# Performance work log

Measured on AMD Instinct MI355X. Metric: run time of the kernel, lower is better.

The kernel has to match this reference:

```python
import jax, jax.numpy as jnp
import numpy as np

MARGIN = 1.0
N, D = 4096, 512
NUM_CLASSES = 64


def setup_inputs() -> dict:
    key = jax.random.key(0)
    k1, k2 = jax.random.split(key)
    inputs = jax.random.normal(k1, (N, D), dtype=jnp.float32)
    targets = jax.random.randint(k2, (N,), 0, NUM_CLASSES, dtype=jnp.int64)
    return {"inputs": inputs, "targets": targets}


def reference(inputs, targets):
    n = inputs.shape[0]
    sq = jnp.sum(inputs * inputs, axis=1)  # [n]
    # squared Euclidean distances, clamped at 0 (matches relu in original)
    d2 = jnp.maximum(sq[:, None] + sq[None, :] - 2.0 * (inputs @ inputs.T), 0.0)
    # safe sqrt (zero entries get 0, matching forward; avoids NaN grads)
    dist = jnp.where(d2 > 0, jnp.sqrt(jnp.where(d2 > 0, d2, 1.0)), 0.0)  # [n,n]

    same = targets[:, None] == targets[None, :]
    eye = jnp.eye(n, dtype=bool)
    pos_mask = same & ~eye          # positives, diagonal excluded
    neg_mask = ~same                # negatives (diagonal is same-label, excluded)

    # per-row sum_k exp(margin - d_ik) over negatives  (replaces per-pair loop)
    neg_sum = jnp.sum(jnp.where(neg_mask, jnp.exp(MARGIN - dist), 0.0), axis=1)  # [n]

    # J_ij = log(neg_sum_i + neg_sum_j) + d_ij for positive pairs
    J = jnp.log(neg_sum[:, None] + neg_sum[None, :]) + dist
    triu_pos = jnp.triu(pos_mask)   # loop iterated over upper-triangular positives
    hinge2 = jnp.where(triu_pos, jax.nn.relu(J) ** 2, 0.0)

    # original divides by count of ALL positive entries (both triangles)
    len_p = jnp.sum(pos_mask).astype(jnp.float32)
    return jnp.sum(hinge2) / len_p
```

## Files before the change

### kernel.cpp

```cpp
#include <hip/hip_runtime.h>
#include <math.h>

#define NN 4096
#define DD 512
#define MARGINF 1.0f
#define NCLS 64
#define MAXM 160
#define TRI (MAXM * (MAXM - 1) / 2)
#define NBLK 2080

typedef __attribute__((ext_vector_type(8))) short bf16x8;
typedef __attribute__((ext_vector_type(4))) float f32x4;

#define WS_SQ   0
#define WS_LOSS 8192
#define WS_CTR  8193
#define WS_LENP 8194
#define WS_RK   8320
#define WS_MEM  12416
#define WS_P    32768
#define WS_XF   557056
#define WS_PD   1605632

__device__ __forceinline__ unsigned short f2bf(float f) {
    unsigned u = __float_as_uint(f);
    u += 0x7fffu + ((u >> 16) & 1u);
    return (unsigned short)(u >> 16);
}

__global__ __launch_bounds__(256) void prep_kernel(const float* __restrict__ X,
                                                   const int* __restrict__ tgt,
                                                   float* __restrict__ ws) {
    __shared__ int tg[NN];
    const int tid = threadIdx.x;
    for (int j = tid; j < NN; j += 256) tg[j] = tgt[j];

    const int wv = tid >> 6, lane = tid & 63;
    const int row = blockIdx.x * 4 + wv;
    const float4* xr = (const float4*)(X + (size_t)row * DD);
    float4 a = xr[2 * lane], b = xr[2 * lane + 1];
    float s = a.x * a.x + a.y * a.y + a.z * a.z + a.w * a.w
            + b.x * b.x + b.y * b.y + b.z * b.z + b.w * b.w;
#pragma unroll
    for (int off = 32; off; off >>= 1) s += __shfl_down(s, off, 64);

    ushort4 pa = {f2bf(a.x), f2bf(a.y), f2bf(a.z), f2bf(a.w)};
    ushort4 pb = {f2bf(b.x), f2bf(b.y), f2bf(b.z), f2bf(b.w)};
    const int r16 = row >> 4, m = row & 15;
    const int kb = lane >> 2, q = lane & 3;
    ushort4* dst = (ushort4*)((unsigned short*)(ws + WS_XF)
                              + ((size_t)(r16 * 16 + kb) * 64 + q * 16 + m) * 8);
    dst[0] = pa;
    dst[1] = pb;

    __syncthreads();
    const int myc = tg[row];
    int cnt = 0;
    for (int j = lane; j < row; j += 64) cnt += (tg[j] == myc) ? 1 : 0;
#pragma unroll
    for (int off = 32; off; off >>= 1) cnt += __shfl_down(cnt, off, 64);
    if (lane == 0) {
        ws[WS_SQ + row] = s;
        ((int*)(ws + WS_RK))[row] = cnt;
        if (cnt < MAXM) ((int*)(ws + WS_MEM))[myc * MAXM + cnt] = row;
    }
    if (blockIdx.x == 0 && tid == 0) {
        ws[WS_LOSS] = 0.0f;
        ((unsigned*)ws)[WS_CTR] = 0u;
        ws[WS_LENP] = 0.0f;
    }
}

__global__ __launch_bounds__(256, 3) void negsum_kernel(const int* __restrict__ tgt,
                                                        float* __restrict__ ws) {
    const int bidx = blockIdx.x;
    int bj = (int)((sqrtf(8.0f * (float)bidx + 1.0f) - 1.0f) * 0.5f);
    while (bj * (bj + 1) / 2 > bidx) --bj;
    while ((bj + 1) * (bj + 2) / 2 <= bidx) ++bj;
    const int bi = bidx - bj * (bj + 1) / 2;
    const int i0 = bi * 64, j0 = bj * 64;

    const int tid = threadIdx.x;
    const int w = tid >> 6, lane = tid & 63;
    const int m_ = lane & 15, q = lane >> 4;
    const int wr = (w & 1) * 32, wc = (w >> 1) * 32;
    const unsigned short* Xf = (const unsigned short*)(ws + WS_XF);

    const int air = (i0 + wr) >> 4;
    const int bjr = (j0 + wc) >> 4;
    const unsigned short* pA = Xf + (size_t)air * 8192 + lane * 8;
    const unsigned short* pB = Xf + (size_t)bjr * 8192 + lane * 8;

    f32x4 acc[2][2] = {};
    bf16x8 cur[4][4], nxt[4][4];
#pragma unroll
    for (int s = 0; s < 4; ++s) {
        cur[s][0] = *(const bf16x8*)(pA + s * 512);
        cur[s][1] = *(const bf16x8*)(pA + 8192 + s * 512);
        cur[s][2] = *(const bf16x8*)(pB + s * 512);
        cur[s][3] = *(const bf16x8*)(pB + 8192 + s * 512);
    }
#pragma unroll
    for (int ch = 0; ch < 4; ++ch) {
        if (ch < 3) {
#pragma unroll
            for (int s = 0; s < 4; ++s) {
                const int it = (ch + 1) * 4 + s;
                nxt[s][0] = *(const bf16x8*)(pA + it * 512);
                nxt[s][1] = *(const bf16x8*)(pA + 8192 + it * 512);
                nxt[s][2] = *(const bf16x8*)(pB + it * 512);
                nxt[s][3] = *(const bf16x8*)(pB + 8192 + it * 512);
            }
        }
#pragma unroll
        for (int s = 0; s < 4; ++s) {
            acc[0][0] = __builtin_amdgcn_mfma_f32_16x16x32_bf16(cur[s][0], cur[s][2], acc[0][0], 0, 0, 0);
            acc[0][1] = __builtin_amdgcn_mfma_f32_16x16x32_bf16(cur[s][0], cur[s][3], acc[0][1], 0, 0, 0);
            acc[1][0] = __builtin_amdgcn_mfma_f32_16x16x32_bf16(cur[s][1], cur[s][2], acc[1][0], 0, 0, 0);
            acc[1][1] = __builtin_amdgcn_mfma_f32_16x16x32_bf16(cur[s][1], cur[s][3], acc[1][1], 0, 0, 0);
        }
#pragma unroll
        for (int s = 0; s < 4; ++s)
#pragma unroll
            for (int f = 0; f < 4; ++f)
                cur[s][f] = nxt[s][f];
    }

    const float* sq = ws + WS_SQ;
    float* P = ws + WS_P;
    const int* rk = (const int*)(ws + WS_RK);
    float* posd = ws + WS_PD;
    const int hrow = wc >> 5;
    const int hcol = wr >> 5;
    float sjv[2]; int tjv[2], jv[2];
#pragma unroll
    for (int v = 0; v < 2; ++v) {
        int j = j0 + wc + v * 16 + m_;
        jv[v] = j;
        sjv[v] = sq[j];
        tjv[v] = tgt[j];
    }
    float colp[2] = {0.0f, 0.0f};
#pragma unroll
    for (int u = 0; u < 2; ++u) {
#pragma unroll
        for (int r = 0; r < 4; ++r) {
            const int i = i0 + wr + u * 16 + q * 4 + r;
            const float si = sq[i];
            const int ti = tgt[i];
            float rp = 0.0f;
#pragma unroll
            for (int v = 0; v < 2; ++v) {
                float d2 = si + sjv[v] - 2.0f * acc[u][v][r];
                float dist = d2 > 0.0f ? sqrtf(d2) : 0.0f;
                if (tjv[v] != ti) {
                    float e = __expf(MARGINF - dist);
                    rp += e;
                    colp[v] += e;
                } else if (i < jv[v]) {
                    int ra = rk[i], rb = rk[jv[v]];
                    if (ra < MAXM && rb < MAXM) {
                        int hi = ra > rb ? ra : rb;
                        int lo = ra > rb ? rb : ra;
                        posd[ti * TRI + hi * (hi - 1) / 2 + lo] = dist;
                    }
                }
            }
            rp += __shfl_xor(rp, 1, 64);
            rp += __shfl_xor(rp, 2, 64);
            rp += __shfl_xor(rp, 4, 64);
            rp += __shfl_xor(rp, 8, 64);
            if (m_ == 0) P[(size_t)i * 128 + bj * 2 + hrow] = rp;
        }
    }
    if (bi != bj) {
#pragma unroll
        for (int v = 0; v < 2; ++v) {
            float cp = colp[v];
            cp += __shfl_xor(cp, 16, 64);
            cp += __shfl_xor(cp, 32, 64);
            if (q == 0) P[(size_t)jv[v] * 128 + bi * 2 + hcol] = cp;
        }
    }
}

__global__ __launch_bounds__(256) void pair2_kernel(const int* __restrict__ tgt,
                                                    float* __restrict__ ws,
                                                    float* __restrict__ out) {
    __shared__ float nsm[MAXM];
    __shared__ float wsum[4];
    __shared__ int csum[4];
    __shared__ bool last;
    const int c = blockIdx.x;
    const int tid = threadIdx.x;
    const int wv = tid >> 6, lane = tid & 63;

    int ccount = 0;
    for (int j = tid; j < NN; j += 256) ccount += (tgt[j] == c) ? 1 : 0;
#pragma unroll
    for (int off = 32; off; off >>= 1) ccount += __shfl_down(ccount, off, 64);
    if (lane == 0) csum[wv] = ccount;
    __syncthreads();
    int mc = csum[0] + csum[1] + csum[2] + csum[3];
    if (mc > MAXM) mc = MAXM;
    const int P_ = mc * (mc - 1) / 2;
    const int* mem = (const int*)(ws + WS_MEM) + c * MAXM;
    const float* Pp = ws + WS_P;

    for (int p = wv; p < mc; p += 4) {
        const float* row = Pp + (size_t)mem[p] * 128;
        float v = row[lane] + row[lane + 64];
#pragma unroll
        for (int off = 32; off; off >>= 1) v += __shfl_xor(v, off, 64);
        if (lane == 0) nsm[p] = v;
    }
    __syncthreads();

    const float* pd = ws + WS_PD + c * TRI;
    float lsum = 0.0f;
    for (int p = tid; p < P_; p += 256) {
        int b = (int)((1.0f + sqrtf(1.0f + 8.0f * (float)p)) * 0.5f);
        while (b * (b - 1) / 2 > p) --b;
        while ((b + 1) * b / 2 <= p) ++b;
        const int a = p - b * (b - 1) / 2;
        const float dist = pd[b * (b - 1) / 2 + a];
        float J = __logf(nsm[a] + nsm[b]) + dist;
        float h = fmaxf(J, 0.0f);
        lsum += h * h;
    }
#pragma unroll
    for (int off = 32; off; off >>= 1) lsum += __shfl_xor(lsum, off, 64);
    if (lane == 0) wsum[wv] = lsum;
    __syncthreads();
    if (tid == 0) {
        float s = wsum[0] + wsum[1] + wsum[2] + wsum[3];
        if (s != 0.0f) atomicAdd(&ws[WS_LOSS], s);
        atomicAdd(&ws[WS_LENP], (float)(mc * (mc - 1)));
        __threadfence();
        unsigned d = atomicAdd((unsigned*)ws + WS_CTR, 1u);
        last = (d == NCLS - 1);
    }
    __syncthreads();
    if (last && tid == 0) {
        float total = atomicAdd(&ws[WS_LOSS], 0.0f);
        float lp = atomicAdd(&ws[WS_LENP], 0.0f);
        out[0] = total / lp;
    }
}

extern "C" void kernel_launch(void* const* d_in, const int* in_sizes, int n_in,
                              void* d_out, int out_size, void* d_ws, size_t ws_size,
                              hipStream_t stream) {
    const float* X  = (const float*)d_in[0];
    const int*  tgt = (const int*)d_in[1];
    float* ws  = (float*)d_ws;
    float* out = (float*)d_out;

    hipLaunchKernelGGL(prep_kernel, dim3(NN / 4), dim3(256), 0, stream, X, tgt, ws);
    hipLaunchKernelGGL(negsum_kernel, dim3(NBLK), dim3(256), 0, stream, tgt, ws);
    hipLaunchKernelGGL(pair2_kernel, dim3(NCLS), dim3(256), 0, stream, tgt, ws, out);
}
```

Before: 121.2 us.

## Fuse per-class pair loss into negsum kernel via last-blocks atomic ticket

Removes the separate pair2 launch. Each negsum block takes an atomic ticket after finishing, and the last 64 blocks to arrive each handle one class's pair loss. Per-class counts are now computed once in the prep kernel instead of each block rescanning all targets. This saves a kernel launch and its tail, but relies on threadfence/atomic ordering for visibility of the P writes from other blocks, and it puts the serial pair work on the tail of the big kernel.

```diff
diff --git a/kernel.cpp b/kernel.cpp
--- a/kernel.cpp
+++ b/kernel.cpp
@@ -16,6 +16,8 @@
 #define WS_LOSS 8192
 #define WS_CTR  8193
 #define WS_LENP 8194
+#define WS_CTR2 8195
+#define WS_CNTC 8196
 #define WS_RK   8320
 #define WS_MEM  12416
 #define WS_P    32768
@@ -64,15 +66,24 @@
         ((int*)(ws + WS_RK))[row] = cnt;
         if (cnt < MAXM) ((int*)(ws + WS_MEM))[myc * MAXM + cnt] = row;
     }
-    if (blockIdx.x == 0 && tid == 0) {
-        ws[WS_LOSS] = 0.0f;
-        ((unsigned*)ws)[WS_CTR] = 0u;
-        ws[WS_LENP] = 0.0f;
+    if (blockIdx.x == 0) {
+        if (tid < NCLS) {
+            int cc = 0;
+            for (int j = 0; j < NN; ++j) cc += (tg[j] == tid) ? 1 : 0;
+            ((int*)(ws + WS_CNTC))[tid] = cc;
+        }
+        if (tid == 0) {
+            ws[WS_LOSS] = 0.0f;
+            ((unsigned*)ws)[WS_CTR] = 0u;
+            ((unsigned*)ws)[WS_CTR2] = 0u;
+            ws[WS_LENP] = 0.0f;
+        }
     }
 }
 
 __global__ __launch_bounds__(256, 3) void negsum_kernel(const int* __restrict__ tgt,
-                                                        float* __restrict__ ws) {
+                                                        float* __restrict__ ws,
+                                                        float* __restrict__ out) {
     const int bidx = blockIdx.x;
     int bj = (int)((sqrtf(8.0f * (float)bidx + 1.0f) - 1.0f) * 0.5f);
     while (bj * (bj + 1) / 2 > bidx) --bj;
@@ -182,32 +193,23 @@
             if (q == 0) P[(size_t)jv[v] * 128 + bi * 2 + hcol] = cp;
         }
     }
-}
-
-__global__ __launch_bounds__(256) void pair2_kernel(const int* __restrict__ tgt,
-                                                    float* __restrict__ ws,
-                                                    float* __restrict__ out) {
+
+    __shared__ unsigned myord;
     __shared__ float nsm[MAXM];
     __shared__ float wsum[4];
-    __shared__ int csum[4];
-    __shared__ bool last;
-    const int c = blockIdx.x;
-    const int tid = threadIdx.x;
-    const int wv = tid >> 6, lane = tid & 63;
-
-    int ccount = 0;
-    for (int j = tid; j < NN; j += 256) ccount += (tgt[j] == c) ? 1 : 0;
-#pragma unroll
-    for (int off = 32; off; off >>= 1) ccount += __shfl_down(ccount, off, 64);
-    if (lane == 0) csum[wv] = ccount;
-    __syncthreads();
-    int mc = csum[0] + csum[1] + csum[2] + csum[3];
+    __threadfence();
+    if (tid == 0) myord = atomicAdd((unsigned*)ws + WS_CTR, 1u);
+    __syncthreads();
+    if (myord < NBLK - NCLS) return;
+    const int c = (int)(myord - (NBLK - NCLS));
+
+    int mc = ((const int*)(ws + WS_CNTC))[c];
     if (mc > MAXM) mc = MAXM;
     const int P_ = mc * (mc - 1) / 2;
     const int* mem = (const int*)(ws + WS_MEM) + c * MAXM;
     const float* Pp = ws + WS_P;
 
-    for (int p = wv; p < mc; p += 4) {
+    for (int p = w; p < mc; p += 4) {
         const float* row = Pp + (size_t)mem[p] * 128;
         float v = row[lane] + row[lane + 64];
 #pragma unroll
@@ -230,14 +232,15 @@
     }
 #pragma unroll
     for (int off = 32; off; off >>= 1) lsum += __shfl_xor(lsum, off, 64);
-    if (lane == 0) wsum[wv] = lsum;
-    __syncthreads();
+    if (lane == 0) wsum[w] = lsum;
+    __syncthreads();
+    __shared__ bool last;
     if (tid == 0) {
         float s = wsum[0] + wsum[1] + wsum[2] + wsum[3];
         if (s != 0.0f) atomicAdd(&ws[WS_LOSS], s);
         atomicAdd(&ws[WS_LENP], (float)(mc * (mc - 1)));
         __threadfence();
-        unsigned d = atomicAdd((unsigned*)ws + WS_CTR, 1u);
+        unsigned d = atomicAdd((unsigned*)ws + WS_CTR2, 1u);
         last = (d == NCLS - 1);
     }
     __syncthreads();
@@ -257,6 +260,5 @@
     float* out = (float*)d_out;
 
     hipLaunchKernelGGL(prep_kernel, dim3(NN / 4), dim3(256), 0, stream, X, tgt, ws);
-    hipLaunchKernelGGL(negsum_kernel, dim3(NBLK), dim3(256), 0, stream, tgt, ws);
-    hipLaunchKernelGGL(pair2_kernel, dim3(NCLS), dim3(256), 0, stream, tgt, ws, out);
-}
+    hipLaunchKernelGGL(negsum_kernel, dim3(NBLK), dim3(256), 0, stream, tgt, ws, out);
+}
```

Measured after the change: 397.9 us. +228.4%, slower.
